# Performance work log

Measured on AMD Instinct MI355X. Metric: run time of the kernel, lower is better.

The kernel has to match this reference:

```python
import jax, jax.numpy as jnp
import numpy as np
import math

B, S, D, H, M = 2, 2048, 1024, 16, 64
HD = D // H  # head_dim = 64


def setup_inputs() -> dict:
    key = jax.random.key(0)
    ks = jax.random.split(key, 16)
    inp = {
        "query": jax.random.normal(ks[0], (B, S, D), jnp.float32),
        "key": jax.random.normal(ks[1], (B, S, D), jnp.float32),
        "value": jax.random.normal(ks[2], (B, S, D), jnp.float32),
        "mask": jax.random.randint(ks[3], (B, 1, 1, S), 0, 2, jnp.int32),
        "Wq": jax.random.normal(ks[4], (D, D), jnp.float32) * 0.02,
        "bq": jnp.zeros((D,), jnp.float32),
        "Wk": jax.random.normal(ks[5], (D, D), jnp.float32) * 0.02,
        "bk": jnp.zeros((D,), jnp.float32),
        "Wv": jax.random.normal(ks[6], (D, D), jnp.float32) * 0.02,
        "bv": jnp.zeros((D,), jnp.float32),
        "Wo": jax.random.normal(ks[7], (D, D), jnp.float32) * 0.02,
        "bo": jnp.zeros((D,), jnp.float32),
        "m_k": jax.random.normal(ks[8], (1, M, D), jnp.float32) * (1.0 / HD),
        "m_v": jax.random.normal(ks[9], (1, M, D), jnp.float32) * (1.0 / M),
    }
    return inp


def reference(query, key, value, mask, Wq, bq, Wk, bk, Wv, bv, Wo, bo, m_k, m_v):
    b, nq, d = query.shape
    nk = key.shape[1]
    h, hd, m = H, HD, M
    scale = math.sqrt(hd)

    Q = query @ Wq.T + bq                      # [b, nq, d]
    K = key @ Wk.T + bk                        # [b, nk, d]
    V = value @ Wv.T + bv                      # [b, nk, d]

    mk = scale * jnp.broadcast_to(m_k, (b, m, d))           # sqrt(head_dim)*m_k
    mv = math.sqrt(m) * jnp.broadcast_to(m_v, (b, m, d))    # sqrt(m)*m_v

    K = jnp.concatenate([K, mk], axis=1)       # [b, nk+m, d]
    V = jnp.concatenate([V, mv], axis=1)

    Qh = Q.reshape(b, nq, h, hd).transpose(0, 2, 1, 3)           # [b,h,nq,hd]
    Kh = K.reshape(b, nk + m, h, hd).transpose(0, 2, 1, 3)       # [b,h,nk+m,hd]
    Vh = V.reshape(b, nk + m, h, hd).transpose(0, 2, 1, 3)

    energy = jnp.einsum('bhqd,bhkd->bhqk', Qh, Kh) / scale       # [b,h,nq,nk+m]
    # mask only the first nk key columns; memory slots are never masked
    masked = jnp.where(mask == 0, jnp.float32(-1e20), energy[..., :nk])
    energy = jnp.concatenate([masked, energy[..., nk:]], axis=-1)

    attention = jax.nn.softmax(energy, axis=-1)
    x = jnp.einsum('bhqk,bhkd->bhqd', attention, Vh)             # [b,h,nq,hd]
    x = x.transpose(0, 2, 1, 3).reshape(b, nq, d)
    return x @ Wo.T + bo
```

## Files before the change

kernel.cpp:

```cpp
#include <hip/hip_runtime.h>
#include <hip/hip_bf16.h>
#include <stdint.h>

#define B_  2
#define S_  2048
#define D_  1024
#define H_  16
#define HD_ 64
#define M_  64
#define SKM (S_ + M_)
#define LOG2E 1.44269504088896340736f

typedef __attribute__((ext_vector_type(8))) short s16x8;
typedef __attribute__((ext_vector_type(4))) float f32x4;
typedef __attribute__((ext_vector_type(16))) float f32x16;

#define GLOAD16(gp, lp) __builtin_amdgcn_global_load_lds( \
    (const __attribute__((address_space(1))) void*)(gp),  \
    (__attribute__((address_space(3))) void*)(lp), 16, 0, 0)

__device__ __forceinline__ unsigned short f2bf(float f) {
  union { float f; unsigned int u; } v; v.f = f;
  unsigned int r = v.u + 0x7fffu + ((v.u >> 16) & 1u);
  return (unsigned short)(r >> 16);
}

__device__ __forceinline__ unsigned pkbf(float lo, float hi) {
  union { __hip_bfloat162 b; unsigned u; } t;
  t.b = __float22bfloat162_rn(make_float2(lo, hi));
  return t.u;
}

__global__ void compact_mask(const int* __restrict__ mask,
                             int* __restrict__ idx, int* __restrict__ cnt) {
  const int b = blockIdx.x;
  __shared__ int base, wsum[4];
  if (threadIdx.x == 0) base = 0;
  const int lane = threadIdx.x & 63, w = threadIdx.x >> 6;
  __syncthreads();
  for (int c = 0; c < S_; c += 256) {
    int key = c + threadIdx.x;
    int mv = mask[b * S_ + key];
    unsigned long long bal = __ballot(mv != 0);
    int pre = __popcll(bal & ((1ull << lane) - 1ull));
    if (lane == 0) wsum[w] = __popcll(bal);
    __syncthreads();
    int woff = 0;
    for (int i = 0; i < w; i++) woff += wsum[i];
    int tot = wsum[0] + wsum[1] + wsum[2] + wsum[3];
    if (mv) idx[b * S_ + base + woff + pre] = key;
    __syncthreads();
    if (threadIdx.x == 0) base += tot;
    __syncthreads();
  }
  if (threadIdx.x == 0) cnt[b] = base;
}

__global__ void cvt_f32_to_bf16(const float* __restrict__ in,
                                unsigned short* __restrict__ out) {
  int i = (blockIdx.x * blockDim.x + threadIdx.x) * 4;
  float4 v = *(const float4*)&in[i];
  ushort4 o;
  o.x = f2bf(v.x); o.y = f2bf(v.y); o.z = f2bf(v.z); o.w = f2bf(v.w);
  *(ushort4*)&out[i] = o;
}

__global__ void cvt_w4(const float* __restrict__ w0, const float* __restrict__ w1,
                       const float* __restrict__ w2, const float* __restrict__ w3,
                       unsigned short* __restrict__ o0, unsigned short* __restrict__ o1,
                       unsigned short* __restrict__ o2, unsigned short* __restrict__ o3) {
  const float* in; unsigned short* out;
  switch (blockIdx.y) {
    case 0: in = w0; out = o0; break;
    case 1: in = w1; out = o1; break;
    case 2: in = w2; out = o2; break;
    default: in = w3; out = o3; break;
  }
  int i = (blockIdx.x * 256 + threadIdx.x) * 4;
  float4 v = *(const float4*)&in[i];
  ushort4 o;
  o.x = f2bf(v.x); o.y = f2bf(v.y); o.z = f2bf(v.z); o.w = f2bf(v.w);
  *(ushort4*)&out[i] = o;
}

__global__ void cvt_kv_gather(const float* __restrict__ key, const float* __restrict__ value,
                              unsigned short* __restrict__ kf, unsigned short* __restrict__ vf,
                              const int* __restrict__ idx, const int* __restrict__ cnt) {
  int b = blockIdx.y, j = blockIdx.x;
  if (j >= cnt[b]) return;
  const float* in = blockIdx.z ? value : key;
  unsigned short* out = blockIdx.z ? vf : kf;
  int src = idx[b * S_ + j];
  const float* ip = in + ((size_t)(b * S_) + src) * D_;
  unsigned short* op = out + ((size_t)(b * S_) + j) * D_;
  int t = threadIdx.x * 4;
  float4 v = *(const float4*)&ip[t];
  ushort4 o;
  o.x = f2bf(v.x); o.y = f2bf(v.y); o.z = f2bf(v.z); o.w = f2bf(v.w);
  *(ushort4*)&op[t] = o;
}

__global__ void fill_mem(const float* __restrict__ mk, const float* __restrict__ mv,
                         unsigned short* __restrict__ Kb, unsigned short* __restrict__ VtG,
                         const int* __restrict__ cnt) {
  int i = blockIdx.x * 256 + threadIdx.x;
  int row = i >> 10, col = i & 1023;
  int hI = col >> 6, dd = col & 63;
  unsigned short kv = f2bf(8.0f * mk[i]);
  unsigned short vv = f2bf(8.0f * mv[i]);
#pragma unroll
  for (int b = 0; b < B_; b++) {
    int c = cnt[b];
    Kb[((size_t)(b * SKM) + c + row) * D_ + col] = kv;
    VtG[((size_t)(b * H_ + hI) * HD_ + dd) * SKM + c + row] = vv;
  }
}

__device__ __forceinline__ void gemm_core(
    const unsigned short* __restrict__ A,
    const unsigned short* __restrict__ Bw,
    unsigned short* As, unsigned short* Bs,
    int mBase, int nBase, int K,
    int w, int lane, int wr, int wc, int lr, int lk,
    f32x4 acc[4][4]) {
  const int sr = lane >> 3, sc = lane & 7;
  for (int k0 = 0; k0 < K; k0 += 64) {
    __syncthreads();
#pragma unroll
    for (int i = 0; i < 4; i++) {
      int r = w * 32 + i * 8 + sr;
      int c = sc ^ (r & 7);
      GLOAD16(&A[(size_t)(mBase + r) * K + k0 + c * 8], &As[(w * 32 + i * 8) * 64]);
      GLOAD16(&Bw[(size_t)(nBase + r) * K + k0 + c * 8], &Bs[(w * 32 + i * 8) * 64]);
    }
    __syncthreads();
#pragma unroll
    for (int ks = 0; ks < 2; ks++) {
      s16x8 af[4], bf[4];
#pragma unroll
      for (int mi = 0; mi < 4; mi++) {
        int row = wr * 64 + mi * 16 + lr;
        af[mi] = *(const s16x8*)&As[row * 64 + (((ks * 4 + lk) ^ (row & 7)) << 3)];
      }
#pragma unroll
      for (int ni = 0; ni < 4; ni++) {
        int row = wc * 64 + ni * 16 + lr;
        bf[ni] = *(const s16x8*)&Bs[row * 64 + (((ks * 4 + lk) ^ (row & 7)) << 3)];
      }
#pragma unroll
      for (int mi = 0; mi < 4; mi++)
#pragma unroll
        for (int ni = 0; ni < 4; ni++)
          acc[mi][ni] = __builtin_amdgcn_mfma_f32_16x16x32_bf16(af[mi], bf[ni], acc[mi][ni], 0, 0, 0);
    }
  }
}

__global__ __launch_bounds__(256)
void gemm_qkv(const unsigned short* __restrict__ qf, const unsigned short* __restrict__ kf,
              const unsigned short* __restrict__ vf,
              const unsigned short* __restrict__ wq, const unsigned short* __restrict__ wk,
              const unsigned short* __restrict__ wv,
              const float* __restrict__ bq, const float* __restrict__ bk,
              const float* __restrict__ bv,
              unsigned short* __restrict__ Qb, unsigned short* __restrict__ Kb,
              unsigned short* __restrict__ Vt,
              const int* __restrict__ cnt) {
  __shared__ __align__(16) unsigned short As[128 * 64];
  __shared__ __align__(16) unsigned short Bs[128 * 64];
  const int z = blockIdx.z;
  const int mBase = blockIdx.y * 128, nBase = blockIdx.x * 128;
  if (z) {
    int c = (mBase < S_) ? cnt[0] : cnt[1];
    int lo = (mBase < S_) ? mBase : (mBase - S_);
    if (lo >= c) return;
  }
  const unsigned short* A  = (z == 0) ? qf : (z == 1) ? kf : vf;
  const unsigned short* Bw = (z == 0) ? wq : (z == 1) ? wk : wv;
  const float* bias        = (z == 0) ? bq : (z == 1) ? bk : bv;

  const int tid = threadIdx.x, lane = tid & 63;
  const int w = tid >> 6, wr = w >> 1, wc = w & 1;
  const int lr = lane & 15, lk = lane >> 4;

  const f32x4 fz = {0.f, 0.f, 0.f, 0.f};
  f32x4 acc[4][4];
#pragma unroll
  for (int i = 0; i < 4; i++)
#pragma unroll
    for (int j = 0; j < 4; j++) acc[i][j] = fz;

  gemm_core(A, Bw, As, Bs, mBase, nBase, D_, w, lane, wr, wc, lr, lk, acc);

  const float alpha = (z == 0) ? 0.125f * LOG2E : 1.0f;
#pragma unroll
  for (int mi = 0; mi < 4; mi++)
#pragma unroll
    for (int ni = 0; ni < 4; ni++)
#pragma unroll
      for (int r = 0; r < 4; r++) {
        int gr = mBase + wr * 64 + mi * 16 + lk * 4 + r;
        int gc = nBase + wc * 64 + ni * 16 + lr;
        float v = (acc[mi][ni][r] + bias[gc]) * alpha;
        if (z == 2) {
          int bb = gr / S_, s = gr - bb * S_;
          int hI = gc >> 6, dd = gc & 63;
          Vt[((size_t)(bb * H_ + hI) * HD_ + dd) * SKM + s] = f2bf(v);
        } else if (z == 1) {
          int orow = gr + (gr / S_) * M_;
          Kb[(size_t)orow * D_ + gc] = f2bf(v);
        } else {
          Qb[(size_t)gr * D_ + gc] = f2bf(v);
        }
      }
}

__global__ __launch_bounds__(256)
void gemm_o(const unsigned short* __restrict__ A, const unsigned short* __restrict__ Bw,
            const float* __restrict__ bias, float* __restrict__ Cout) {
  __shared__ __align__(16) unsigned short As[128 * 64];
  __shared__ __align__(16) unsigned short Bs[128 * 64];
  const int mBase = blockIdx.y * 128, nBase = blockIdx.x * 128;
  const int tid = threadIdx.x, lane = tid & 63;
  const int w = tid >> 6, wr = w >> 1, wc = w & 1;
  const int lr = lane & 15, lk = lane >> 4;

  const f32x4 fz = {0.f, 0.f, 0.f, 0.f};
  f32x4 acc[4][4];
#pragma unroll
  for (int i = 0; i < 4; i++)
#pragma unroll
    for (int j = 0; j < 4; j++) acc[i][j] = fz;

  gemm_core(A, Bw, As, Bs, mBase, nBase, D_, w, lane, wr, wc, lr, lk, acc);

#pragma unroll
  for (int mi = 0; mi < 4; mi++)
#pragma unroll
    for (int ni = 0; ni < 4; ni++)
#pragma unroll
      for (int r = 0; r < 4; r++) {
        int gr = mBase + wr * 64 + mi * 16 + lk * 4 + r;
        int gc = nBase + wc * 64 + ni * 16 + lr;
        Cout[(size_t)gr * D_ + gc] = acc[mi][ni][r] + bias[gc];
      }
}

__global__ __launch_bounds__(256)
void attn_kernel(const unsigned short* __restrict__ Qb,
                 const unsigned short* __restrict__ Kb,
                 const unsigned short* __restrict__ VtG,
                 const int* __restrict__ cnt,
                 unsigned short* __restrict__ Xb) {
  __shared__ __align__(16) unsigned short Ks[64 * 64];
  __shared__ __align__(16) unsigned short Vs[64 * 64];

  const int tid = threadIdx.x, lane = tid & 63, w = tid >> 6;
  const int l31 = lane & 31, hh = lane >> 5;
  const int qt = blockIdx.x, h = blockIdx.y, b = blockIdx.z;

  const int total = cnt[b] + M_;
  const int nt = (total + 63) >> 6;

  const int r0 = tid >> 3, c0 = tid & 7;
  const int ck = c0 ^ (r0 & 7);
  const unsigned short* Kg = Kb + (size_t)b * SKM * D_ + (size_t)h * HD_;
  const unsigned short* Vg = VtG + (size_t)(b * H_ + h) * HD_ * SKM;

  const unsigned short* qp = Qb + ((size_t)(b * S_) + qt * 128 + w * 32 + l31) * D_ + h * HD_;
  s16x8 qf[4];
#pragma unroll
  for (int ds = 0; ds < 4; ds++) qf[ds] = *(const s16x8*)&qp[ds * 16 + hh * 8];

  f32x16 accO[2];
#pragma unroll
  for (int dt = 0; dt < 2; dt++)
#pragma unroll
    for (int j = 0; j < 16; j++) accO[dt][j] = 0.f;
  float m_r = -1e20f, l_r = 0.f;

  uint4 kr0, kr1, vr0, vr1;
  auto LOAD = [&](int kt) {
    kr0 = *(const uint4*)&Kg[(size_t)(kt * 64 + r0) * D_ + c0 * 8];
    kr1 = *(const uint4*)&Kg[(size_t)(kt * 64 + r0 + 32) * D_ + c0 * 8];
    vr0 = *(const uint4*)&Vg[(size_t)r0 * SKM + kt * 64 + c0 * 8];
    vr1 = *(const uint4*)&Vg[(size_t)(r0 + 32) * SKM + kt * 64 + c0 * 8];
  };
  LOAD(0);

  for (int kt = 0; kt < nt; ++kt) {
    __syncthreads();
    *(uint4*)&Ks[r0 * 64 + ck * 8] = kr0;
    *(uint4*)&Ks[(r0 + 32) * 64 + ck * 8] = kr1;
    *(uint4*)&Vs[r0 * 64 + ck * 8] = vr0;
    *(uint4*)&Vs[(r0 + 32) * 64 + ck * 8] = vr1;
    __syncthreads();
    if (kt + 1 < nt) LOAD(kt + 1);

    f32x16 p0, p1;
#pragma unroll
    for (int j = 0; j < 16; j++) { p0[j] = 0.f; p1[j] = 0.f; }
#pragma unroll
    for (int ds = 0; ds < 4; ds++) {
      s16x8 ka0 = *(const s16x8*)&Ks[l31 * 64 + (((ds * 2 + hh) ^ (l31 & 7)) << 3)];
      s16x8 ka1 = *(const s16x8*)&Ks[(32 + l31) * 64 + (((ds * 2 + hh) ^ (l31 & 7)) << 3)];
      p0 = __builtin_amdgcn_mfma_f32_32x32x16_bf16(ka0, qf[ds], p0, 0, 0, 0);
      p1 = __builtin_amdgcn_mfma_f32_32x32x16_bf16(ka1, qf[ds], p1, 0, 0, 0);
    }

    if (kt == nt - 1) {
      int valid = total - kt * 64;
#pragma unroll
      for (int j = 0; j < 16; j++) {
        int kl = (j & 3) + 8 * (j >> 2) + 4 * hh;
        if (kl >= valid) p0[j] = -1e30f;
        if (kl + 32 >= valid) p1[j] = -1e30f;
      }
    }

    float vmax = fmaxf(p0[0], p1[0]);
#pragma unroll
    for (int j = 1; j < 16; j++) vmax = fmaxf(vmax, fmaxf(p0[j], p1[j]));
    vmax = fmaxf(vmax, __shfl_xor(vmax, 32));
    if (!__all(vmax - m_r <= 8.0f)) {
      float mnew = fmaxf(m_r, vmax);
      float fac = __builtin_amdgcn_exp2f(m_r - mnew);
      m_r = mnew;
      l_r *= fac;
#pragma unroll
      for (int dt = 0; dt < 2; dt++)
#pragma unroll
        for (int j = 0; j < 16; j++) accO[dt][j] *= fac;
    }
    float sum = 0.f;
#pragma unroll
    for (int j = 0; j < 16; j++) {
      p0[j] = __builtin_amdgcn_exp2f(p0[j] - m_r); sum += p0[j];
      p1[j] = __builtin_amdgcn_exp2f(p1[j] - m_r); sum += p1[j];
    }
    sum += __shfl_xor(sum, 32);
    l_r += sum;

    s16x8 pf_[4];
#pragma unroll
    for (int ks = 0; ks < 4; ks++) {
      const int base = (ks & 1) * 8;
#define ELT(t) ((ks >= 2) ? p1[base + (t)] : p0[base + (t)])
      unsigned w0 = pkbf(ELT(0), ELT(1));
      unsigned w1 = pkbf(ELT(2), ELT(3));
      unsigned w2 = pkbf(ELT(4), ELT(5));
      unsigned w3 = pkbf(ELT(6), ELT(7));
#undef ELT
      unsigned s0 = hh ? w0 : w2;
      unsigned s1 = hh ? w1 : w3;
      unsigned g0 = (unsigned)__shfl_xor((int)s0, 32);
      unsigned g1 = (unsigned)__shfl_xor((int)s1, 32);
      union { s16x8 v; unsigned u[4]; } pf;
      pf.u[0] = hh ? g0 : w0;
      pf.u[1] = hh ? g1 : w1;
      pf.u[2] = hh ? w2 : g0;
      pf.u[3] = hh ? w3 : g1;
      pf_[ks] = pf.v;
    }

#pragma unroll
    for (int dt = 0; dt < 2; dt++)
#pragma unroll
      for (int ks = 0; ks < 4; ks++) {
        s16x8 va = *(const s16x8*)&Vs[(dt * 32 + l31) * 64 + (((ks * 2 + hh) ^ (l31 & 7)) << 3)];
        accO[dt] = __builtin_amdgcn_mfma_f32_32x32x16_bf16(va, pf_[ks], accO[dt], 0, 0, 0);
      }
  }

  float invl = 1.0f / l_r;
  size_t orow = ((size_t)(b * S_) + qt * 128 + w * 32 + l31) * D_ + h * HD_;
#pragma unroll
  for (int dt = 0; dt < 2; dt++)
#pragma unroll
    for (int j = 0; j < 16; j++) {
      int d = dt * 32 + (j & 3) + 8 * (j >> 2) + 4 * hh;
      Xb[orow + d] = f2bf(accO[dt][j] * invl);
    }
}

extern "C" void kernel_launch(void* const* d_in, const int* in_sizes, int n_in,
                              void* d_out, int out_size, void* d_ws, size_t ws_size,
                              hipStream_t stream) {
  const float* query = (const float*)d_in[0];
  const float* key   = (const float*)d_in[1];
  const float* value = (const float*)d_in[2];
  const int*   mask  = (const int*)d_in[3];
  const float* Wq    = (const float*)d_in[4];
  const float* bq    = (const float*)d_in[5];
  const float* Wk    = (const float*)d_in[6];
  const float* bk    = (const float*)d_in[7];
  const float* Wv    = (const float*)d_in[8];
  const float* bv    = (const float*)d_in[9];
  const float* Wo    = (const float*)d_in[10];
  const float* bo    = (const float*)d_in[11];
  const float* m_k   = (const float*)d_in[12];
  const float* m_v   = (const float*)d_in[13];

  const int NQ = B_ * S_ * D_;
  const int NW = D_ * D_;
  const int NK = B_ * SKM * D_;

  unsigned short* ws = (unsigned short*)d_ws;
  unsigned short* qf = ws;
  unsigned short* kf = qf + NQ;
  unsigned short* vf = kf + NQ;
  unsigned short* wq = vf + NQ;
  unsigned short* wk = wq + NW;
  unsigned short* wv = wk + NW;
  unsigned short* wo = wv + NW;
  unsigned short* Qb = wo + NW;
  unsigned short* Kb = Qb + NQ;
  unsigned short* Vt = Kb + NK;
  unsigned short* Xb = Vt + NK;
  int* idx = (int*)(Xb + NQ);
  int* cnt = idx + B_ * S_;

  compact_mask<<<B_, 256, 0, stream>>>(mask, idx, cnt);
  cvt_f32_to_bf16<<<NQ / 1024, 256, 0, stream>>>(query, qf);
  cvt_kv_gather<<<dim3(S_, B_, 2), 256, 0, stream>>>(key, value, kf, vf, idx, cnt);
  cvt_w4<<<dim3(NW / 1024, 4), 256, 0, stream>>>(Wq, Wk, Wv, Wo, wq, wk, wv, wo);

  gemm_qkv<<<dim3(D_ / 128, (B_ * S_) / 128, 3), 256, 0, stream>>>(
      qf, kf, vf, wq, wk, wv, bq, bk, bv, Qb, Kb, Vt, cnt);
  fill_mem<<<(M_ * D_) / 256, 256, 0, stream>>>(m_k, m_v, Kb, Vt, cnt);

  attn_kernel<<<dim3(S_ / 128, H_, B_), 256, 0, stream>>>(Qb, Kb, Vt, cnt, Xb);

  gemm_o<<<dim3(D_ / 128, (B_ * S_) / 128), 256, 0, stream>>>(Xb, wo, bo, (float*)d_out);
}
```

Before: 146.7 us.

## Double-buffer GEMM LDS tiles with K=32 stages and remap block order for L2 reuse

New measurement: 144.8 us, median of 2. Within noise of the previous version (-1.3%).

```diff
diff --git a/kernel.cpp b/kernel.cpp
--- a/kernel.cpp
+++ b/kernel.cpp
@@ -116,44 +116,55 @@
   }
 }
 
-__device__ __forceinline__ void gemm_core(
+__device__ __forceinline__ void gemm_core2(
     const unsigned short* __restrict__ A,
     const unsigned short* __restrict__ Bw,
     unsigned short* As, unsigned short* Bs,
     int mBase, int nBase, int K,
     int w, int lane, int wr, int wc, int lr, int lk,
     f32x4 acc[4][4]) {
-  const int sr = lane >> 3, sc = lane & 7;
-  for (int k0 = 0; k0 < K; k0 += 64) {
-    __syncthreads();
-#pragma unroll
-    for (int i = 0; i < 4; i++) {
-      int r = w * 32 + i * 8 + sr;
-      int c = sc ^ (r & 7);
-      GLOAD16(&A[(size_t)(mBase + r) * K + k0 + c * 8], &As[(w * 32 + i * 8) * 64]);
-      GLOAD16(&Bw[(size_t)(nBase + r) * K + k0 + c * 8], &Bs[(w * 32 + i * 8) * 64]);
-    }
-    __syncthreads();
-#pragma unroll
-    for (int ks = 0; ks < 2; ks++) {
-      s16x8 af[4], bf[4];
-#pragma unroll
-      for (int mi = 0; mi < 4; mi++) {
-        int row = wr * 64 + mi * 16 + lr;
-        af[mi] = *(const s16x8*)&As[row * 64 + (((ks * 4 + lk) ^ (row & 7)) << 3)];
-      }
-#pragma unroll
-      for (int ni = 0; ni < 4; ni++) {
-        int row = wc * 64 + ni * 16 + lr;
-        bf[ni] = *(const s16x8*)&Bs[row * 64 + (((ks * 4 + lk) ^ (row & 7)) << 3)];
-      }
-#pragma unroll
-      for (int mi = 0; mi < 4; mi++)
-#pragma unroll
-        for (int ni = 0; ni < 4; ni++)
-          acc[mi][ni] = __builtin_amdgcn_mfma_f32_16x16x32_bf16(af[mi], bf[ni], acc[mi][ni], 0, 0, 0);
-    }
-  }
+  const int srow = w * 32 + (lane >> 2);
+  const int cd = lane & 3;
+  const int NT = K / 32;
+
+#define STAGE_(buf, k0)                                                          \
+  {                                                                              \
+    _Pragma("unroll")                                                            \
+    for (int i = 0; i < 2; i++) {                                                \
+      int r = srow + i * 16;                                                     \
+      int ca = cd ^ ((r >> 1) & 3);           \
+      GLOAD16(&A[(size_t)(mBase + r) * K + (k0) + ca * 8],                       \
+              &As[(buf) * (128 * 32) + (w * 32 + i * 16) * 32]);                 \
+      GLOAD16(&Bw[(size_t)(nBase + r) * K + (k0) + ca * 8],                      \
+              &Bs[(buf) * (128 * 32) + (w * 32 + i * 16) * 32]);                 \
+    }                                                                            \
+  }
+
+  STAGE_(0, 0);
+  __syncthreads();
+  int cur = 0;
+  for (int t = 0; t < NT; ++t) {
+    if (t + 1 < NT) STAGE_(cur ^ 1, (t + 1) * 32);
+    s16x8 af[4], bf[4];
+#pragma unroll
+    for (int mi = 0; mi < 4; mi++) {
+      int row = wr * 64 + mi * 16 + lr;
+      af[mi] = *(const s16x8*)&As[cur * (128 * 32) + row * 32 + ((lk ^ ((row >> 1) & 3)) << 3)];
+    }
+#pragma unroll
+    for (int ni = 0; ni < 4; ni++) {
+      int row = wc * 64 + ni * 16 + lr;
+      bf[ni] = *(const s16x8*)&Bs[cur * (128 * 32) + row * 32 + ((lk ^ ((row >> 1) & 3)) << 3)];
+    }
+#pragma unroll
+    for (int mi = 0; mi < 4; mi++)
+#pragma unroll
+      for (int ni = 0; ni < 4; ni++)
+        acc[mi][ni] = __builtin_amdgcn_mfma_f32_16x16x32_bf16(af[mi], bf[ni], acc[mi][ni], 0, 0, 0);
+    __syncthreads();
+    cur ^= 1;
+  }
+#undef STAGE_
 }
 
 __global__ __launch_bounds__(256)
@@ -166,10 +177,12 @@
               unsigned short* __restrict__ Qb, unsigned short* __restrict__ Kb,
               unsigned short* __restrict__ Vt,
               const int* __restrict__ cnt) {
-  __shared__ __align__(16) unsigned short As[128 * 64];
-  __shared__ __align__(16) unsigned short Bs[128 * 64];
-  const int z = blockIdx.z;
-  const int mBase = blockIdx.y * 128, nBase = blockIdx.x * 128;
+  __shared__ __align__(16) unsigned short As[2 * 128 * 32];
+  __shared__ __align__(16) unsigned short Bs[2 * 128 * 32];
+  const int z = blockIdx.x >> 8;
+  const int local = blockIdx.x & 255;
+  const int ws = (local & 7) * 32 + (local >> 3);
+  const int nBase = (ws & 7) * 128, mBase = (ws >> 3) * 128;
   if (z) {
     int c = (mBase < S_) ? cnt[0] : cnt[1];
     int lo = (mBase < S_) ? mBase : (mBase - S_);
@@ -190,7 +203,7 @@
 #pragma unroll
     for (int j = 0; j < 4; j++) acc[i][j] = fz;
 
-  gemm_core(A, Bw, As, Bs, mBase, nBase, D_, w, lane, wr, wc, lr, lk, acc);
+  gemm_core2(A, Bw, As, Bs, mBase, nBase, D_, w, lane, wr, wc, lr, lk, acc);
 
   const float alpha = (z == 0) ? 0.125f * LOG2E : 1.0f;
 #pragma unroll
@@ -218,9 +231,11 @@
 __global__ __launch_bounds__(256)
 void gemm_o(const unsigned short* __restrict__ A, const unsigned short* __restrict__ Bw,
             const float* __restrict__ bias, float* __restrict__ Cout) {
-  __shared__ __align__(16) unsigned short As[128 * 64];
-  __shared__ __align__(16) unsigned short Bs[128 * 64];
-  const int mBase = blockIdx.y * 128, nBase = blockIdx.x * 128;
+  __shared__ __align__(16) unsigned short As[2 * 128 * 32];
+  __shared__ __align__(16) unsigned short Bs[2 * 128 * 32];
+  const int local = blockIdx.x & 255;
+  const int ws = (local & 7) * 32 + (local >> 3);
+  const int nBase = (ws & 7) * 128, mBase = (ws >> 3) * 128;
   const int tid = threadIdx.x, lane = tid & 63;
   const int w = tid >> 6, wr = w >> 1, wc = w & 1;
   const int lr = lane & 15, lk = lane >> 4;
@@ -232,7 +247,7 @@
 #pragma unroll
     for (int j = 0; j < 4; j++) acc[i][j] = fz;
 
-  gemm_core(A, Bw, As, Bs, mBase, nBase, D_, w, lane, wr, wc, lr, lk, acc);
+  gemm_core2(A, Bw, As, Bs, mBase, nBase, D_, w, lane, wr, wc, lr, lk, acc);
 
 #pragma unroll
   for (int mi = 0; mi < 4; mi++)
@@ -425,11 +440,10 @@
   cvt_kv_gather<<<dim3(S_, B_, 2), 256, 0, stream>>>(key, value, kf, vf, idx, cnt);
   cvt_w4<<<dim3(NW / 1024, 4), 256, 0, stream>>>(Wq, Wk, Wv, Wo, wq, wk, wv, wo);
 
-  gemm_qkv<<<dim3(D_ / 128, (B_ * S_) / 128, 3), 256, 0, stream>>>(
-      qf, kf, vf, wq, wk, wv, bq, bk, bv, Qb, Kb, Vt, cnt);
+  gemm_qkv<<<768, 256, 0, stream>>>(qf, kf, vf, wq, wk, wv, bq, bk, bv, Qb, Kb, Vt, cnt);
   fill_mem<<<(M_ * D_) / 256, 256, 0, stream>>>(m_k, m_v, Kb, Vt, cnt);
 
   attn_kernel<<<dim3(S_ / 128, H_, B_), 256, 0, stream>>>(Qb, Kb, Vt, cnt, Xb);
 
-  gemm_o<<<dim3(D_ / 128, (B_ * S_) / 128), 256, 0, stream>>>(Xb, wo, bo, (float*)d_out);
-}
+  gemm_o<<<256, 256, 0, stream>>>(Xb, wo, bo, (float*)d_out);
+}
```
